# Optimization experiments

Hardware: AMD Instinct MI355X
Metric: run time of the kernel (lower is better)

Reference implementation:

```python
import math
import jax, jax.numpy as jnp
import numpy as np

HEADS = 16
REL_WINDOW = 128


def setup_inputs() -> dict:
    key = jax.random.key(0)
    k1, k2, k3, k4, k5 = jax.random.split(key, 5)
    b, s, d = 2, 2048, 1024
    hd = d // HEADS          # 64
    R = 2 * REL_WINDOW + 1   # 257
    return {
        "x": jax.random.normal(k1, (b, s, d), dtype=jnp.float32),
        "Wqkv": jax.random.normal(k2, (3 * d, d), dtype=jnp.float32) * (1.0 / math.sqrt(d)),
        "bqkv": jax.random.normal(k3, (3 * d,), dtype=jnp.float32) * 0.02,
        "Wr": jax.random.normal(k4, (R, hd), dtype=jnp.float32) * (1.0 / math.sqrt(hd)),
        "br": jax.random.normal(k5, (R,), dtype=jnp.float32) * 0.02,
    }


def reference(x, Wqkv, bqkv, Wr, br):
    b, s, d = x.shape
    h = HEADS
    hd = d // h
    w = REL_WINDOW
    scale = math.sqrt(d / h)

    # qkv projection; torch view(b,s,h,3*hd) then chunk(3, dim=-1)
    qkv = (x @ Wqkv.T + bqkv).reshape(b, s, h, 3 * hd)
    q, k, v = jnp.split(qkv, 3, axis=-1)          # each [b,s,h,hd]
    q = q.transpose(0, 2, 1, 3)                   # [b,h,s,hd]
    k = k.transpose(0, 2, 1, 3)
    v = v.transpose(0, 2, 1, 3)

    # content scores
    content = jnp.einsum('bhik,bhjk->bhij', q, k) / scale  # [b,h,s,s]

    # relative position scores: project queries to R logits, gather per (i,j) offset
    idx = jnp.arange(s)
    offsets = jnp.clip(idx[None, :] - idx[:, None], -w, w) + w  # [s,s] in [0, 2w]
    rp = jnp.einsum('bhik,rk->bhir', q, Wr) + br               # [b,h,s,R]
    pos = jnp.take_along_axis(rp, jnp.broadcast_to(offsets, (b, h, s, s)), axis=-1)

    attn = jax.nn.softmax(content + pos, axis=-1)
    out = jnp.einsum('bhij,bhjk->bhik', attn, v)  # [b,h,s,hd]
    return out.transpose(0, 2, 1, 3).reshape(b, s, d)
```

## Files before the change

kernel.cpp:

```cpp
#include <hip/hip_runtime.h>

typedef short bfrag __attribute__((ext_vector_type(8)));
typedef float f32x4 __attribute__((ext_vector_type(4)));

#define MFMA16(a, b, c) __builtin_amdgcn_mfma_f32_16x16x32_bf16((a), (b), (c), 0, 0, 0)

#define SEQ   2048
#define DMOD  1024
#define NHEAD 16
#define HDIM  64
#define RSZ   257
#define RSTRIDE 260
#define RPADN 272
#define XN    (4096*1024)
#define WN    (3072*1024)
#define LOG2E 1.44269504f

__device__ __forceinline__ unsigned short f2bf(float f) {
  unsigned int u = __float_as_uint(f);
  u += 0x7FFFu + ((u >> 16) & 1u);
  return (unsigned short)(u >> 16);
}
__device__ __forceinline__ float bf2f(unsigned short u) {
  return __uint_as_float(((unsigned int)u) << 16);
}
__device__ __forceinline__ unsigned int pkbf(float a, float b) {
#if defined(__gfx950__)
  unsigned int r;
  asm("v_cvt_pk_bf16_f32 %0, %1, %2" : "=v"(r) : "v"(a), "v"(b));
  return r;
#else
  return (unsigned int)f2bf(a) | ((unsigned int)f2bf(b) << 16);
#endif
}
__device__ __forceinline__ float fexp2(float x) {
#if __has_builtin(__builtin_amdgcn_exp2f)
  return __builtin_amdgcn_exp2f(x);
#else
  return __expf(x * 0.69314718f);
#endif
}
__device__ __forceinline__ void gl2lds16(const void* g, void* l) {
  __builtin_amdgcn_global_load_lds(
      (__attribute__((address_space(1))) void*)(g),
      (__attribute__((address_space(3))) void*)(l), 16, 0, 0);
}

__global__ __launch_bounds__(256) void cast_all(const float* __restrict__ x,
                                                const float* __restrict__ Wqkv,
                                                const float* __restrict__ Wr,
                                                unsigned short* __restrict__ xb,
                                                unsigned short* __restrict__ wb,
                                                unsigned short* __restrict__ wrb) {
  int i = (blockIdx.x * 256 + threadIdx.x) * 4;
  if (i < XN) {
    float4 v = *(const float4*)(x + i);
    ushort4 o; o.x = f2bf(v.x); o.y = f2bf(v.y); o.z = f2bf(v.z); o.w = f2bf(v.w);
    *(ushort4*)(xb + i) = o;
  } else if (i < XN + WN) {
    int j = i - XN;
    float4 v = *(const float4*)(Wqkv + j);
    ushort4 o; o.x = f2bf(v.x); o.y = f2bf(v.y); o.z = f2bf(v.z); o.w = f2bf(v.w);
    *(ushort4*)(wb + j) = o;
  } else {
    int j = i - XN - WN;
    ushort4 o;
    unsigned short t[4];
#pragma unroll
    for (int k = 0; k < 4; ++k)
      t[k] = (j + k < RSZ * HDIM) ? f2bf(Wr[j + k]) : (unsigned short)0;
    o.x = t[0]; o.y = t[1]; o.z = t[2]; o.w = t[3];
    *(ushort4*)(wrb + j) = o;
  }
}

__global__ __launch_bounds__(256) void qkv_gemm(const unsigned short* __restrict__ xb,
                                                const unsigned short* __restrict__ wb,
                                                const float* __restrict__ bqkv,
                                                unsigned short* __restrict__ qb,
                                                unsigned short* __restrict__ kbuf,
                                                unsigned short* __restrict__ vtb) {
  __shared__ unsigned short SMEM[2 * 128 * 64];
  unsigned short* As = SMEM;
  unsigned short* Bs = SMEM + 128 * 64;
  unsigned short* Vtmp = SMEM;
  const int tid = threadIdx.x;
  const int m0 = blockIdx.y * 128, n0 = blockIdx.x * 128;
  const int wave = tid >> 6, lane = tid & 63;
  const int q4 = lane >> 4, l16 = lane & 15;
  const int wm = (wave & 1) * 64, wn = (wave >> 1) * 64;
  const int sw = l16 & 7;

  f32x4 acc[4][4];
#pragma unroll
  for (int rt = 0; rt < 4; ++rt)
#pragma unroll
    for (int ct = 0; ct < 4; ++ct) acc[rt][ct] = (f32x4){0.f, 0.f, 0.f, 0.f};

  for (int k0 = 0; k0 < DMOD; k0 += 64) {
#pragma unroll
    for (int it = 0; it < 4; ++it) {
      int ch = it * 256 + tid;
      int r = ch >> 3, cl = (ch & 7) ^ (r & 7);
      gl2lds16(xb + (size_t)(m0 + r) * DMOD + k0 + cl * 8, As + ch * 8);
      gl2lds16(wb + (size_t)(n0 + r) * DMOD + k0 + cl * 8, Bs + ch * 8);
    }
    __syncthreads();
#pragma unroll
    for (int ks = 0; ks < 2; ++ks) {
      bfrag af[4], bf[4];
#pragma unroll
      for (int rt = 0; rt < 4; ++rt)
        af[rt] = *(const bfrag*)(As + (wm + rt * 16 + l16) * 64 + ((ks * 4 + q4) ^ sw) * 8);
#pragma unroll
      for (int ct = 0; ct < 4; ++ct)
        bf[ct] = *(const bfrag*)(Bs + (wn + ct * 16 + l16) * 64 + ((ks * 4 + q4) ^ sw) * 8);
#pragma unroll
      for (int rt = 0; rt < 4; ++rt)
#pragma unroll
        for (int ct = 0; ct < 4; ++ct)
          acc[rt][ct] = MFMA16(bf[ct], af[rt], acc[rt][ct]);
    }
    __syncthreads();
  }

  const int batch = m0 >> 11;
  const int sbase = m0 & 2047;
  const int r3 = blockIdx.x % 3;
  const bool hasV = (r3 != 0);
  const int nv0 = n0 + ((r3 == 2) ? 64 : 0);

#pragma unroll
  for (int ct = 0; ct < 4; ++ct) {
    int ng = n0 + wn + ct * 16 + q4 * 4;
    int hh = ng / 192;
    int rem = ng - hh * 192;
    int t = rem >> 6, dd = rem & 63;
    float4 b4 = *(const float4*)(bqkv + ng);
    if (t < 2) {
      unsigned short* dst = (t == 0) ? qb : kbuf;
      size_t rowo = ((size_t)(batch * NHEAD + hh)) * SEQ + sbase;
#pragma unroll
      for (int rt = 0; rt < 4; ++rt) {
        int m = wm + rt * 16 + l16;
        uint2 pv;
        pv.x = pkbf(acc[rt][ct][0] + b4.x, acc[rt][ct][1] + b4.y);
        pv.y = pkbf(acc[rt][ct][2] + b4.z, acc[rt][ct][3] + b4.w);
        *(uint2*)(dst + (rowo + m) * HDIM + dd) = pv;
      }
    } else {
#pragma unroll
      for (int rt = 0; rt < 4; ++rt) {
        int m = wm + rt * 16 + l16;
        Vtmp[(dd + 0) * 136 + m] = f2bf(acc[rt][ct][0] + b4.x);
        Vtmp[(dd + 1) * 136 + m] = f2bf(acc[rt][ct][1] + b4.y);
        Vtmp[(dd + 2) * 136 + m] = f2bf(acc[rt][ct][2] + b4.z);
        Vtmp[(dd + 3) * 136 + m] = f2bf(acc[rt][ct][3] + b4.w);
      }
    }
  }

  if (hasV) {
    __syncthreads();
    const int hh = nv0 / 192;
    unsigned short* vdst = vtb + ((size_t)(batch * NHEAD + hh)) * HDIM * SEQ;
#pragma unroll
    for (int it = 0; it < 4; ++it) {
      int u = it * 256 + tid;
      int dd = u >> 4, mc = u & 15;
      bfrag val = *(const bfrag*)(Vtmp + dd * 136 + mc * 8);
      *(bfrag*)(vdst + (size_t)dd * SEQ + sbase + mc * 8) = val;
    }
  }
}

__global__ __launch_bounds__(256) void rp_gemm(const unsigned short* __restrict__ qb,
                                               const unsigned short* __restrict__ wrb,
                                               const float* __restrict__ br,
                                               unsigned short* __restrict__ rp16) {
  __shared__ unsigned short WrS[RPADN * HDIM];
  __shared__ unsigned short Qs[64 * HDIM];
  const int tid = threadIdx.x;
  const size_t row0 = (size_t)blockIdx.x * 64;

  for (int i = tid; i < RPADN * HDIM / 8; i += 256)
    *(uint4*)(&WrS[i * 8]) = *(const uint4*)(&wrb[i * 8]);
  for (int i = tid; i < 512; i += 256)
    *(uint4*)(&Qs[i * 8]) = *(const uint4*)(&qb[row0 * HDIM + i * 8]);
  __syncthreads();

  const int wave = tid >> 6, lane = tid & 63;
  const int q4 = lane >> 4, l16 = lane & 15;

  bfrag af0 = *(const bfrag*)(Qs + (wave * 16 + l16) * 64 + q4 * 8);
  bfrag af1 = *(const bfrag*)(Qs + (wave * 16 + l16) * 64 + 32 + q4 * 8);

  unsigned short* rrow = rp16 + (row0 + wave * 16 + l16) * RSTRIDE;
  const float br256 = br[256];

#pragma unroll 4
  for (int ct = 0; ct < 16; ++ct) {
    f32x4 acc = (f32x4){0.f, 0.f, 0.f, 0.f};
    bfrag w0 = *(const bfrag*)(WrS + (ct * 16 + l16) * 64 + q4 * 8);
    bfrag w1 = *(const bfrag*)(WrS + (ct * 16 + l16) * 64 + 32 + q4 * 8);
    acc = MFMA16(w0, af0, acc);
    acc = MFMA16(w1, af1, acc);
    int r = ct * 16 + q4 * 4;
    float4 b4 = *(const float4*)(br + r);
    uint2 pv;
    pv.x = pkbf((acc[0] + b4.x) * LOG2E, (acc[1] + b4.y) * LOG2E);
    pv.y = pkbf((acc[2] + b4.z) * LOG2E, (acc[3] + b4.w) * LOG2E);
    *(uint2*)(rrow + r) = pv;
  }
  {
    f32x4 acc = (f32x4){0.f, 0.f, 0.f, 0.f};
    bfrag w0 = *(const bfrag*)(WrS + (256 + l16) * 64 + q4 * 8);
    bfrag w1 = *(const bfrag*)(WrS + (256 + l16) * 64 + 32 + q4 * 8);
    acc = MFMA16(w0, af0, acc);
    acc = MFMA16(w1, af1, acc);
    if (q4 == 0)
      rrow[256] = f2bf((acc[0] + br256) * LOG2E);
  }
}

__global__ __launch_bounds__(256) void flash_attn(const unsigned short* __restrict__ qb,
                                                  const unsigned short* __restrict__ kbuf,
                                                  const unsigned short* __restrict__ vtb,
                                                  const unsigned short* __restrict__ rp16,
                                                  float* __restrict__ out) {
  __shared__ unsigned short Ks[64 * 64];
  __shared__ unsigned short Vs[64 * 64];
  __shared__ unsigned short Ps[64 * 64];

  const int tid = threadIdx.x;
  const int i0 = blockIdx.x * 64;
  const int bh = blockIdx.y;
  const int wave = tid >> 6, lane = tid & 63;
  const int q4 = lane >> 4, l16 = lane & 15;
  const int sw = l16 & 7;
  const float SC = 0.125f * LOG2E;

  const int rloc = wave * 16 + l16;
  const int ig = i0 + rloc;
  const unsigned short* qrow = qb + ((size_t)bh * SEQ + ig) * HDIM;
  bfrag qf0 = *(const bfrag*)(qrow + q4 * 8);
  bfrag qf1 = *(const bfrag*)(qrow + 32 + q4 * 8);

  const unsigned short* rpbase = rp16 + ((size_t)bh * SEQ + ig) * RSTRIDE;
  const float rpL = bf2f(rpbase[0]);
  const float rpR = bf2f(rpbase[256]);

  float m_s = -3.0e38f, l_s = 0.f;
  f32x4 oacc[4];
#pragma unroll
  for (int ct = 0; ct < 4; ++ct) oacc[ct] = (f32x4){0.f, 0.f, 0.f, 0.f};

  const unsigned short* kbase = kbuf + (size_t)bh * SEQ * HDIM;
  const unsigned short* vbase = vtb + (size_t)bh * HDIM * SEQ;

  for (int jt = 0; jt < 32; ++jt) {
    const int j0 = jt * 64;
#pragma unroll
    for (int it = 0; it < 2; ++it) {
      int ch = it * 256 + tid;
      int r = ch >> 3, cl = (ch & 7) ^ (r & 7);
      gl2lds16(kbase + (size_t)(j0 + r) * HDIM + cl * 8, Ks + ch * 8);
      gl2lds16(vbase + (size_t)r * SEQ + j0 + cl * 8, Vs + ch * 8);
    }
    __syncthreads();

    f32x4 sacc[4];
#pragma unroll
    for (int ct = 0; ct < 4; ++ct) {
      sacc[ct] = (f32x4){0.f, 0.f, 0.f, 0.f};
      bfrag k0f = *(const bfrag*)(Ks + (ct * 16 + l16) * 64 + (q4 ^ sw) * 8);
      bfrag k1f = *(const bfrag*)(Ks + (ct * 16 + l16) * 64 + ((4 + q4) ^ sw) * 8);
      sacc[ct] = MFMA16(k0f, qf0, sacc[ct]);
      sacc[ct] = MFMA16(k1f, qf1, sacc[ct]);
    }

    float p[4][4];
    const int dj = j0 - i0;
    if (dj >= 191) {
#pragma unroll
      for (int ct = 0; ct < 4; ++ct)
#pragma unroll
        for (int reg = 0; reg < 4; ++reg)
          p[ct][reg] = sacc[ct][reg] * SC + rpR;
    } else if (dj <= -191) {
#pragma unroll
      for (int ct = 0; ct < 4; ++ct)
#pragma unroll
        for (int reg = 0; reg < 4; ++reg)
          p[ct][reg] = sacc[ct][reg] * SC + rpL;
    } else {
#pragma unroll
      for (int ct = 0; ct < 4; ++ct) {
#pragma unroll
        for (int reg = 0; reg < 4; ++reg) {
          int j = j0 + ct * 16 + q4 * 4 + reg;
          int off = j - ig;
          off = (off < -128) ? -128 : (off > 128 ? 128 : off);
          p[ct][reg] = sacc[ct][reg] * SC + bf2f(rpbase[off + 128]);
        }
      }
    }

    float mm;
    {
      float a0 = fmaxf(fmaxf(p[0][0], p[0][1]), fmaxf(p[0][2], p[0][3]));
      float a1 = fmaxf(fmaxf(p[1][0], p[1][1]), fmaxf(p[1][2], p[1][3]));
      float a2 = fmaxf(fmaxf(p[2][0], p[2][1]), fmaxf(p[2][2], p[2][3]));
      float a3 = fmaxf(fmaxf(p[3][0], p[3][1]), fmaxf(p[3][2], p[3][3]));
      mm = fmaxf(fmaxf(a0, a1), fmaxf(a2, a3));
      mm = fmaxf(mm, __shfl_xor(mm, 16));
      mm = fmaxf(mm, __shfl_xor(mm, 32));
    }
    const float mnew = fmaxf(m_s, mm);
    const float alpha = fexp2(m_s - mnew);
    m_s = mnew;
#pragma unroll
    for (int ct = 0; ct < 4; ++ct)
#pragma unroll
      for (int reg = 0; reg < 4; ++reg)
        p[ct][reg] = fexp2(p[ct][reg] - m_s);
    {
      float s0 = (p[0][0] + p[0][1]) + (p[0][2] + p[0][3]);
      float s1 = (p[1][0] + p[1][1]) + (p[1][2] + p[1][3]);
      float s2 = (p[2][0] + p[2][1]) + (p[2][2] + p[2][3]);
      float s3 = (p[3][0] + p[3][1]) + (p[3][2] + p[3][3]);
      float rs = (s0 + s1) + (s2 + s3);
      rs += __shfl_xor(rs, 16);
      rs += __shfl_xor(rs, 32);
      l_s = l_s * alpha + rs;
    }
#pragma unroll
    for (int ct = 0; ct < 4; ++ct)
#pragma unroll
      for (int reg = 0; reg < 4; ++reg)
        oacc[ct][reg] *= alpha;

    unsigned int* Pw = (unsigned int*)Ps;
#pragma unroll
    for (int ct = 0; ct < 4; ++ct) {
      unsigned int pk01 = pkbf(p[ct][0], p[ct][1]);
      unsigned int pk23 = pkbf(p[ct][2], p[ct][3]);
      int chunk = ct * 2 + (q4 >> 1);
      unsigned int a = rloc * 32 + ((chunk ^ sw) << 2) + ((q4 & 1) << 1);
      Pw[a] = pk01;
      Pw[a + 1] = pk23;
    }

    bfrag pf0 = *(const bfrag*)(Ps + rloc * 64 + (q4 ^ sw) * 8);
    bfrag pf1 = *(const bfrag*)(Ps + rloc * 64 + ((4 + q4) ^ sw) * 8);
#pragma unroll
    for (int ct = 0; ct < 4; ++ct) {
      bfrag v0f = *(const bfrag*)(Vs + (ct * 16 + l16) * 64 + (q4 ^ sw) * 8);
      bfrag v1f = *(const bfrag*)(Vs + (ct * 16 + l16) * 64 + ((4 + q4) ^ sw) * 8);
      oacc[ct] = MFMA16(v0f, pf0, oacc[ct]);
      oacc[ct] = MFMA16(v1f, pf1, oacc[ct]);
    }
    __syncthreads();
  }

  const int bidx = bh >> 4, hh = bh & 15;
  const float inv = 1.0f / l_s;
  float* orow = out + ((size_t)bidx * SEQ + ig) * DMOD + hh * HDIM;
#pragma unroll
  for (int ct = 0; ct < 4; ++ct) {
    float4 v;
    v.x = oacc[ct][0] * inv;
    v.y = oacc[ct][1] * inv;
    v.z = oacc[ct][2] * inv;
    v.w = oacc[ct][3] * inv;
    *(float4*)(orow + ct * 16 + q4 * 4) = v;
  }
}

extern "C" void kernel_launch(void* const* d_in, const int* in_sizes, int n_in,
                              void* d_out, int out_size, void* d_ws, size_t ws_size,
                              hipStream_t stream) {
  const float* x    = (const float*)d_in[0];
  const float* Wqkv = (const float*)d_in[1];
  const float* bqkv = (const float*)d_in[2];
  const float* Wr   = (const float*)d_in[3];
  const float* br   = (const float*)d_in[4];
  float* out = (float*)d_out;

  char* ws = (char*)d_ws;
  unsigned short* xb   = (unsigned short*)(ws);
  unsigned short* wb   = (unsigned short*)(ws + 8388608);
  unsigned short* qb   = (unsigned short*)(ws + 14680064);
  unsigned short* kb   = (unsigned short*)(ws + 23068672);
  unsigned short* vtb  = (unsigned short*)(ws + 31457280);
  unsigned short* wrb  = (unsigned short*)(ws + 39845888);
  unsigned short* rp16 = (unsigned short*)(ws + 39880704);

  cast_all<<<7185, 256, 0, stream>>>(x, Wqkv, Wr, xb, wb, wrb);
  qkv_gemm<<<dim3(24, 32), 256, 0, stream>>>(xb, wb, bqkv, qb, kb, vtb);
  rp_gemm<<<1024, 256, 0, stream>>>(qb, wrb, br, rp16);
  flash_attn<<<dim3(32, 32), 256, 0, stream>>>(qb, kb, vtb, rp16, out);
}
```

Measured before the change: 223.8 us.

## Double-buffer K/V tiles, remap blocks for XCD locality, lazy softmax rescale

```diff
diff --git a/kernel.cpp b/kernel.cpp
--- a/kernel.cpp
+++ b/kernel.cpp
@@ -228,13 +228,15 @@
                                                   const unsigned short* __restrict__ vtb,
                                                   const unsigned short* __restrict__ rp16,
                                                   float* __restrict__ out) {
-  __shared__ unsigned short Ks[64 * 64];
-  __shared__ unsigned short Vs[64 * 64];
+  __shared__ unsigned short Ks[2][64 * 64];
+  __shared__ unsigned short Vs[2][64 * 64];
   __shared__ unsigned short Ps[64 * 64];
 
   const int tid = threadIdx.x;
-  const int i0 = blockIdx.x * 64;
-  const int bh = blockIdx.y;
+  const int orig = blockIdx.x;
+  const int slot = orig >> 3;
+  const int bh = (orig & 7) * 4 + (slot >> 5);
+  const int i0 = (slot & 31) << 6;
   const int wave = tid >> 6, lane = tid & 63;
   const int q4 = lane >> 4, l16 = lane & 15;
   const int sw = l16 & 7;
@@ -258,26 +260,43 @@
   const unsigned short* kbase = kbuf + (size_t)bh * SEQ * HDIM;
   const unsigned short* vbase = vtb + (size_t)bh * HDIM * SEQ;
 
-  for (int jt = 0; jt < 32; ++jt) {
-    const int j0 = jt * 64;
+  auto STAGE = [&](int jt, int buf) {
+    const int j0s = jt * 64;
 #pragma unroll
     for (int it = 0; it < 2; ++it) {
       int ch = it * 256 + tid;
       int r = ch >> 3, cl = (ch & 7) ^ (r & 7);
-      gl2lds16(kbase + (size_t)(j0 + r) * HDIM + cl * 8, Ks + ch * 8);
-      gl2lds16(vbase + (size_t)r * SEQ + j0 + cl * 8, Vs + ch * 8);
-    }
-    __syncthreads();
+      gl2lds16(kbase + (size_t)(j0s + r) * HDIM + cl * 8, &Ks[buf][ch * 8]);
+      gl2lds16(vbase + (size_t)r * SEQ + j0s + cl * 8, &Vs[buf][ch * 8]);
+    }
+  };
+
+  STAGE(0, 0);
+
+  for (int jt = 0; jt < 32; ++jt) {
+    const int cur = jt & 1;
+    const int j0 = jt * 64;
+
+    if (jt < 31) {
+      STAGE(jt + 1, cur ^ 1);
+      asm volatile("s_waitcnt vmcnt(4)" ::: "memory");
+    } else {
+      asm volatile("s_waitcnt vmcnt(0)" ::: "memory");
+    }
+    __builtin_amdgcn_s_barrier();
+    asm volatile("" ::: "memory");
 
     f32x4 sacc[4];
+    __builtin_amdgcn_s_setprio(1);
 #pragma unroll
     for (int ct = 0; ct < 4; ++ct) {
       sacc[ct] = (f32x4){0.f, 0.f, 0.f, 0.f};
-      bfrag k0f = *(const bfrag*)(Ks + (ct * 16 + l16) * 64 + (q4 ^ sw) * 8);
-      bfrag k1f = *(const bfrag*)(Ks + (ct * 16 + l16) * 64 + ((4 + q4) ^ sw) * 8);
+      bfrag k0f = *(const bfrag*)(&Ks[cur][(ct * 16 + l16) * 64 + (q4 ^ sw) * 8]);
+      bfrag k1f = *(const bfrag*)(&Ks[cur][(ct * 16 + l16) * 64 + ((4 + q4) ^ sw) * 8]);
       sacc[ct] = MFMA16(k0f, qf0, sacc[ct]);
       sacc[ct] = MFMA16(k1f, qf1, sacc[ct]);
     }
+    __builtin_amdgcn_s_setprio(0);
 
     float p[4][4];
     const int dj = j0 - i0;
@@ -316,9 +335,17 @@
       mm = fmaxf(mm, __shfl_xor(mm, 16));
       mm = fmaxf(mm, __shfl_xor(mm, 32));
     }
-    const float mnew = fmaxf(m_s, mm);
-    const float alpha = fexp2(m_s - mnew);
-    m_s = mnew;
+    if (!__all(mm <= m_s + 8.0f)) {
+      const float mnew = fmaxf(m_s, mm);
+      const float alpha = fexp2(m_s - mnew);
+      m_s = mnew;
+      l_s *= alpha;
+#pragma unroll
+      for (int ct = 0; ct < 4; ++ct)
+#pragma unroll
+        for (int reg = 0; reg < 4; ++reg)
+          oacc[ct][reg] *= alpha;
+    }
 #pragma unroll
     for (int ct = 0; ct < 4; ++ct)
 #pragma unroll
@@ -332,13 +359,8 @@
       float rs = (s0 + s1) + (s2 + s3);
       rs += __shfl_xor(rs, 16);
       rs += __shfl_xor(rs, 32);
-      l_s = l_s * alpha + rs;
-    }
-#pragma unroll
-    for (int ct = 0; ct < 4; ++ct)
-#pragma unroll
-      for (int reg = 0; reg < 4; ++reg)
-        oacc[ct][reg] *= alpha;
+      l_s += rs;
+    }
 
     unsigned int* Pw = (unsigned int*)Ps;
 #pragma unroll
@@ -353,14 +375,18 @@
 
     bfrag pf0 = *(const bfrag*)(Ps + rloc * 64 + (q4 ^ sw) * 8);
     bfrag pf1 = *(const bfrag*)(Ps + rloc * 64 + ((4 + q4) ^ sw) * 8);
+    __builtin_amdgcn_s_setprio(1);
 #pragma unroll
     for (int ct = 0; ct < 4; ++ct) {
-      bfrag v0f = *(const bfrag*)(Vs + (ct * 16 + l16) * 64 + (q4 ^ sw) * 8);
-      bfrag v1f = *(const bfrag*)(Vs + (ct * 16 + l16) * 64 + ((4 + q4) ^ sw) * 8);
+      bfrag v0f = *(const bfrag*)(&Vs[cur][(ct * 16 + l16) * 64 + (q4 ^ sw) * 8]);
+      bfrag v1f = *(const bfrag*)(&Vs[cur][(ct * 16 + l16) * 64 + ((4 + q4) ^ sw) * 8]);
       oacc[ct] = MFMA16(v0f, pf0, oacc[ct]);
       oacc[ct] = MFMA16(v1f, pf1, oacc[ct]);
     }
-    __syncthreads();
+    __builtin_amdgcn_s_setprio(0);
+
+    __builtin_amdgcn_s_barrier();
+    asm volatile("" ::: "memory");
   }
 
   const int bidx = bh >> 4, hh = bh & 15;
@@ -399,5 +425,5 @@
   cast_all<<<7185, 256, 0, stream>>>(x, Wqkv, Wr, xb, wb, wrb);
   qkv_gemm<<<dim3(24, 32), 256, 0, stream>>>(xb, wb, bqkv, qb, kb, vtb);
   rp_gemm<<<1024, 256, 0, stream>>>(qb, wrb, br, rp16);
-  flash_attn<<<dim3(32, 32), 256, 0, stream>>>(qb, kb, vtb, rp16, out);
-}
+  flash_attn<<<1024, 256, 0, stream>>>(qb, kb, vtb, rp16, out);
+}
```

After: 243.3 us. 1.09x slower.
